# Optimization experiments

Measured on AMD Instinct MI355X. Metric: run time of the kernel, lower is better.

Reference implementation:

```python
import jax, jax.numpy as jnp
import numpy as np

N_NODES = 100000
N_EDGES = 3200000
NDIM_IN = 64
EDIM = 64
NDIM_OUT = 32
HID1, HID2 = 50, 25


def _linear_init(key, fan_in, fan_out):
    # torch nn.Linear default: U(-1/sqrt(fan_in), 1/sqrt(fan_in))
    kw, kb = jax.random.split(key)
    bound = 1.0 / np.sqrt(fan_in)
    W = jax.random.uniform(kw, (fan_in, fan_out), jnp.float32, -bound, bound)
    b = jax.random.uniform(kb, (fan_out,), jnp.float32, -bound, bound)
    return W, b


def setup_inputs() -> dict:
    key = jax.random.key(0)
    ks = jax.random.split(key, 10)
    nfeats = jax.random.normal(ks[0], (N_NODES, 1, NDIM_IN), jnp.float32)
    efeats = jax.random.normal(ks[1], (N_EDGES, 1, EDIM), jnp.float32)
    src = jax.random.randint(ks[2], (N_EDGES,), 0, N_NODES, jnp.int32)
    dst = jax.random.randint(ks[3], (N_EDGES,), 0, N_NODES, jnp.int32)
    Wm1, bm1 = _linear_init(ks[4], NDIM_IN + EDIM, HID1)
    Wa1, ba1 = _linear_init(ks[5], NDIM_IN + HID1, HID1)
    Wm2, bm2 = _linear_init(ks[6], HID1 + EDIM, HID2)
    Wa2, ba2 = _linear_init(ks[7], HID1 + HID2, HID2)
    Wm3, bm3 = _linear_init(ks[8], HID2 + EDIM, NDIM_OUT)
    Wa3, ba3 = _linear_init(ks[9], HID2 + NDIM_OUT, NDIM_OUT)
    return {
        "nfeats": nfeats, "efeats": efeats, "src": src, "dst": dst,
        "Wm1": Wm1, "bm1": bm1, "Wa1": Wa1, "ba1": ba1,
        "Wm2": Wm2, "bm2": bm2, "Wa2": Wa2, "ba2": ba2,
        "Wm3": Wm3, "bm3": bm3, "Wa3": Wa3, "ba3": ba3,
    }


def _gnn_layer(h, e, src, dst, Wm, bm, Wa, ba):
    # h: [N,1,Fin], e: [E,1,Fe]
    # per-edge message: relu(Linear(cat(h[src], e)))  -> [E,1,Fout]
    m = jax.nn.relu(jnp.concatenate([h[src], e], axis=-1) @ Wm + bm)
    # sum-aggregate messages per destination node -> [N,1,Fout]
    h_neigh = jax.ops.segment_sum(m, dst, num_segments=h.shape[0])
    # node apply: relu(Linear(cat(h, h_neigh)))
    return jax.nn.relu(jnp.concatenate([h, h_neigh], axis=-1) @ Wa + ba)


def reference(nfeats, efeats, src, dst,
              Wm1, bm1, Wa1, ba1,
              Wm2, bm2, Wa2, ba2,
              Wm3, bm3, Wa3, ba3):
    h = _gnn_layer(nfeats, efeats, src, dst, Wm1, bm1, Wa1, ba1)
    h = _gnn_layer(h, efeats, src, dst, Wm2, bm2, Wa2, ba2)  # dropout p=0.0
    h = _gnn_layer(h, efeats, src, dst, Wm3, bm3, Wa3, ba3)
    return h.sum(axis=1)  # [N, ndim_out]
```

## Files before the change

kernel.cpp:

```cpp
#include <hip/hip_runtime.h>

#define DEVINL __device__ __forceinline__

typedef __attribute__((ext_vector_type(8))) short bf16x8;
typedef __attribute__((ext_vector_type(4))) float f32x4;

DEVINL void fma4(float4& a, const float4 w, const float x) {
    a.x += w.x * x; a.y += w.y * x; a.z += w.z * x; a.w += w.w * x;
}

DEVINL unsigned short bf16of(float x) {
    unsigned a = __float_as_uint(x);
    a += 0x7FFFu + ((a >> 16) & 1u);
    return (unsigned short)(a >> 16);
}

DEVINL unsigned bfpair(float lo, float hi) {
    unsigned a = __float_as_uint(lo);
    a += 0x7FFFu + ((a >> 16) & 1u);
    unsigned b = __float_as_uint(hi);
    b += 0x7FFFu + ((b >> 16) & 1u);
    return (a >> 16) | (b & 0xFFFF0000u);
}

DEVINL bf16x8 as_bf16x8(uint4 u) {
    union { uint4 u4; bf16x8 b; } cv; cv.u4 = u; return cv.b;
}

__global__ __launch_bounds__(256) void hist_kernel(const int* __restrict__ d,
                                                   int* __restrict__ counts, int n) {
    for (int i = blockIdx.x * 256 + threadIdx.x; i < n; i += gridDim.x * 256)
        atomicAdd(&counts[d[i]], 1);
}

__global__ __launch_bounds__(1024) void scan_block(const int* __restrict__ in,
                                                   int* __restrict__ out,
                                                   int* __restrict__ bsums, int n) {
    __shared__ int buf[2][1024];
    const int t = threadIdx.x;
    const int i = blockIdx.x * 1024 + t;
    const int v = (i < n) ? in[i] : 0;
    int cur = 0;
    buf[0][t] = v;
    __syncthreads();
    #pragma unroll
    for (int s = 1; s < 1024; s <<= 1) {
        int x = buf[cur][t];
        if (t >= s) x += buf[cur][t - s];
        buf[cur ^ 1][t] = x;
        cur ^= 1;
        __syncthreads();
    }
    if (i < n) out[i] = buf[cur][t] - v;
    if (t == 1023) bsums[blockIdx.x] = buf[cur][t];
}

__global__ void scan_small(int* __restrict__ bs, int nb) {
    if (blockIdx.x == 0 && threadIdx.x == 0) {
        int acc = 0;
        for (int i = 0; i < nb; i++) { int v = bs[i]; bs[i] = acc; acc += v; }
    }
}

__global__ __launch_bounds__(1024) void add_offsets(int* __restrict__ out,
                                                    const int* __restrict__ bs, int n) {
    int i = blockIdx.x * 1024 + threadIdx.x;
    if (i < n) out[i] += bs[blockIdx.x];
}

__global__ __launch_bounds__(256) void scatter_kernel(const int* __restrict__ d,
                                                      const int* __restrict__ src,
                                                      int* __restrict__ cursor,
                                                      int4* __restrict__ recs, int n) {
    for (int i = blockIdx.x * 256 + threadIdx.x; i < n; i += gridDim.x * 256) {
        int dd = d[i];
        int ss = src[i];
        int pos = atomicAdd(&cursor[dd], 1);
        recs[pos] = make_int4(i, dd, ss, 0);
    }
}

template<int FIN, int FOUT, int FOUTP>
__global__ __launch_bounds__(256) void pack_we(const float* __restrict__ W,
                                               float* __restrict__ Wp) {
    int idx = blockIdx.x * 256 + threadIdx.x;
    if (idx >= 64 * FOUTP) return;
    int k = idx / FOUTP, j = idx - k * FOUTP;
    Wp[idx] = (j < FOUT) ? W[(FIN + k) * FOUT + j] : 0.f;
}

template<int FIN, int FOUT, int NC>
__global__ __launch_bounds__(256) void pack_wbt(const float* __restrict__ W,
                                                unsigned short* __restrict__ WbT) {
    int idx = blockIdx.x * 256 + threadIdx.x;
    if (idx >= NC * 64) return;
    int c = idx / 64, k = idx - c * 64;
    WbT[idx] = (c < FOUT) ? bf16of(W[(FIN + k) * FOUT + c]) : (unsigned short)0;
}

template<int FIN, int FOUT, int FOUTP>
__global__ __launch_bounds__(256) void gemv_g(
    const float* __restrict__ x,
    const float* __restrict__ W,
    const float* __restrict__ b,
    float* __restrict__ g, int nNodes)
{
    constexpr int F4 = FOUTP / 4;
    __shared__ float4 Wl[FIN * F4];
    __shared__ float  bl[FOUTP];
    const int tid = threadIdx.x;
    for (int idx = tid; idx < FIN * FOUTP; idx += 256) {
        int k = idx / FOUTP, j = idx - k * FOUTP;
        reinterpret_cast<float*>(Wl)[idx] = (j < FOUT) ? W[k * FOUT + j] : 0.f;
    }
    for (int idx = tid; idx < FOUTP; idx += 256)
        bl[idx] = (idx < FOUT) ? b[idx] : 0.f;
    __syncthreads();
    const int n = blockIdx.x * 256 + tid;
    if (n >= nNodes) return;
    float4 acc[F4];
    #pragma unroll
    for (int j4 = 0; j4 < F4; j4++) acc[j4] = reinterpret_cast<float4*>(bl)[j4];
    const float* xr = x + (long long)n * FIN;
    #pragma unroll 1
    for (int k = 0; k < FIN; ++k) {
        float xk = xr[k];
        const float4* wrow = &Wl[k * F4];
        #pragma unroll
        for (int j4 = 0; j4 < F4; j4++) fma4(acc[j4], wrow[j4], xk);
    }
    float4* gr = reinterpret_cast<float4*>(g + (long long)n * FOUTP);
    #pragma unroll
    for (int j4 = 0; j4 < F4; j4++) gr[j4] = acc[j4];
}


template<int FOUT, int FOUTP, int NT>
__global__ __launch_bounds__(256) void edge_mfma_cvt(
    const float* __restrict__ g,
    const float* __restrict__ efeats,
    const int4* __restrict__ recs,
    const unsigned short* __restrict__ WbT,
    unsigned* __restrict__ ebf,
    float* __restrict__ agg)
{
    constexpr int MS = NT * 16 + 1;

    __shared__ float msg[4][32 * MS];
    __shared__ int eidL[512], sIdxL[512], dseg[512];

    const int tid = threadIdx.x;
    const long long pb = (long long)blockIdx.x * 512;
    {
        int4 r0 = recs[pb + tid];
        int4 r1 = recs[pb + 256 + tid];
        eidL[tid] = r0.x;  dseg[tid] = r0.y;  sIdxL[tid] = r0.z;
        eidL[tid + 256] = r1.x; dseg[tid + 256] = r1.y; sIdxL[tid + 256] = r1.z;
    }
    __syncthreads();

    const int lane = tid & 63;
    const int wv   = tid >> 6;
    const int lg   = lane >> 4;
    const int lc   = lane & 15;

    bf16x8 bfr[2][NT];
    #pragma unroll
    for (int kt = 0; kt < 2; kt++)
        #pragma unroll
        for (int nt = 0; nt < NT; nt++)
            bfr[kt][nt] = *reinterpret_cast<const bf16x8*>(
                WbT + (nt * 16 + lc) * 64 + kt * 32 + lg * 8);

    float* msgW = msg[wv];

    #pragma unroll 1
    for (int ch = 0; ch < 4; ++ch) {
        const int rb0 = wv * 128 + ch * 32;
        #pragma unroll
        for (int mt = 0; mt < 2; ++mt) {
            const int rowbase = rb0 + mt * 16;
            const int eid = eidL[rowbase + lc];
            const float4* erow = reinterpret_cast<const float4*>(efeats + (long long)eid * 64);
            float4 f0 = erow[lg * 2];
            float4 f1 = erow[lg * 2 + 1];
            float4 f2 = erow[8 + lg * 2];
            float4 f3 = erow[8 + lg * 2 + 1];
            uint4 u0, u1;
            u0.x = bfpair(f0.x, f0.y); u0.y = bfpair(f0.z, f0.w);
            u0.z = bfpair(f1.x, f1.y); u0.w = bfpair(f1.z, f1.w);
            u1.x = bfpair(f2.x, f2.y); u1.y = bfpair(f2.z, f2.w);
            u1.z = bfpair(f3.x, f3.y); u1.w = bfpair(f3.z, f3.w);
            uint4* eb = reinterpret_cast<uint4*>(ebf + (unsigned long long)(pb + rowbase + lc) * 32);
            eb[lg]     = u0;
            eb[4 + lg] = u1;
            bf16x8 a0 = as_bf16x8(u0);
            bf16x8 a1 = as_bf16x8(u1);

            int sr[4];
            #pragma unroll
            for (int r = 0; r < 4; r++) sr[r] = sIdxL[rowbase + lg * 4 + r];
            #pragma unroll
            for (int nt = 0; nt < NT; nt++) {
                f32x4 acc = {0.f, 0.f, 0.f, 0.f};
                acc = __builtin_amdgcn_mfma_f32_16x16x32_bf16(a0, bfr[0][nt], acc, 0, 0, 0);
                acc = __builtin_amdgcn_mfma_f32_16x16x32_bf16(a1, bfr[1][nt], acc, 0, 0, 0);
                const int col = nt * 16 + lc;
                #pragma unroll
                for (int r = 0; r < 4; r++) {
                    float gv = (col < FOUT) ? g[(long long)sr[r] * FOUTP + col] : 0.f;
                    float v  = fmaxf(acc[r] + gv, 0.f);
                    msgW[(mt * 16 + lg * 4 + r) * MS + col] = v;
                }
            }
        }
        const int base = rb0;
        for (int r0 = 0; r0 < 32; ++r0) {
            int dr = dseg[base + r0];
            if (r0 > 0 && dseg[base + r0 - 1] == dr) continue;
            float s = 0.f;
            int rr = r0;
            while (true) {
                s += msgW[rr * MS + lane];
                ++rr;
                if (rr >= 32 || dseg[base + rr] != dr) break;
            }
            if (lane < FOUT) atomicAdd(agg + (long long)dr * FOUT + lane, s);
        }
    }
}

template<int FOUT, int FOUTP, int NT>
__global__ __launch_bounds__(256) void edge_mfma(
    const float* __restrict__ g,
    const unsigned* __restrict__ ebf,
    const int4* __restrict__ recs,
    const unsigned short* __restrict__ WbT,
    float* __restrict__ agg)
{
    constexpr int MS = NT * 16 + 1;

    __shared__ float msg[4][32 * MS];
    __shared__ int sIdxL[512], dseg[512];

    const int tid = threadIdx.x;
    const long long pb = (long long)blockIdx.x * 512;
    {
        int4 r0 = recs[pb + tid];
        int4 r1 = recs[pb + 256 + tid];
        dseg[tid] = r0.y;  sIdxL[tid] = r0.z;
        dseg[tid + 256] = r1.y; sIdxL[tid + 256] = r1.z;
    }
    __syncthreads();

    const int lane = tid & 63;
    const int wv   = tid >> 6;
    const int lg   = lane >> 4;
    const int lc   = lane & 15;

    bf16x8 bfr[2][NT];
    #pragma unroll
    for (int kt = 0; kt < 2; kt++)
        #pragma unroll
        for (int nt = 0; nt < NT; nt++)
            bfr[kt][nt] = *reinterpret_cast<const bf16x8*>(
                WbT + (nt * 16 + lc) * 64 + kt * 32 + lg * 8);

    float* msgW = msg[wv];

    #pragma unroll 1
    for (int ch = 0; ch < 4; ++ch) {
        const int rb0 = wv * 128 + ch * 32;
        #pragma unroll
        for (int mt = 0; mt < 2; ++mt) {
            const int rowbase = rb0 + mt * 16;
            const unsigned* arow = ebf + (unsigned long long)(pb + rowbase + lc) * 32;
            bf16x8 a0 = *reinterpret_cast<const bf16x8*>(arow + lg * 4);
            bf16x8 a1 = *reinterpret_cast<const bf16x8*>(arow + 16 + lg * 4);
            int sr[4];
            #pragma unroll
            for (int r = 0; r < 4; r++) sr[r] = sIdxL[rowbase + lg * 4 + r];
            #pragma unroll
            for (int nt = 0; nt < NT; nt++) {
                f32x4 acc = {0.f, 0.f, 0.f, 0.f};
                acc = __builtin_amdgcn_mfma_f32_16x16x32_bf16(a0, bfr[0][nt], acc, 0, 0, 0);
                acc = __builtin_amdgcn_mfma_f32_16x16x32_bf16(a1, bfr[1][nt], acc, 0, 0, 0);
                const int col = nt * 16 + lc;
                #pragma unroll
                for (int r = 0; r < 4; r++) {
                    float gv = (col < FOUT) ? g[(long long)sr[r] * FOUTP + col] : 0.f;
                    float v  = fmaxf(acc[r] + gv, 0.f);
                    msgW[(mt * 16 + lg * 4 + r) * MS + col] = v;
                }
            }
        }
        const int base = rb0;
        for (int r0 = 0; r0 < 32; ++r0) {
            int dr = dseg[base + r0];
            if (r0 > 0 && dseg[base + r0 - 1] == dr) continue;
            float s = 0.f;
            int rr = r0;
            while (true) {
                s += msgW[rr * MS + lane];
                ++rr;
                if (rr >= 32 || dseg[base + rr] != dr) break;
            }
            if (lane < FOUT) atomicAdd(agg + (long long)dr * FOUT + lane, s);
        }
    }
}

template<int FOUT, int FOUTP, int MS>
__global__ __launch_bounds__(256) void edge_fb(
    const float* __restrict__ g,
    const float* __restrict__ efeats,
    const int4* __restrict__ recs,
    const float* __restrict__ Wp,
    float* __restrict__ agg)
{
    constexpr int F4 = FOUTP / 4;
    constexpr int ST = 17;
    static_assert(128 * MS + 64 <= 512 * ST, "msg buf exceeds sbuf");

    __shared__ float sbuf[512 * ST];
    __shared__ int   dseg[512];

    const int tid = threadIdx.x;
    const long long pb = (long long)blockIdx.x * 512;
    int4 r0 = recs[pb + tid];
    int4 r1 = recs[pb + 256 + tid];
    dseg[tid] = r0.y;
    dseg[tid + 256] = r1.y;

    const float4* gr0 = reinterpret_cast<const float4*>(g + (long long)r0.z * FOUTP);
    const float4* gr1 = reinterpret_cast<const float4*>(g + (long long)r1.z * FOUTP);
    const float*  er0 = efeats + (long long)r0.x * 64;
    const float*  er1 = efeats + (long long)r1.x * 64;
    const float4* Wp4 = reinterpret_cast<const float4*>(Wp);

    float4 acc0[F4], acc1[F4];
    #pragma unroll
    for (int j4 = 0; j4 < F4; j4++) acc0[j4] = gr0[j4];
    #pragma unroll
    for (int j4 = 0; j4 < F4; j4++) acc1[j4] = gr1[j4];

    const int t0 = tid * ST;
    const int t1 = (tid + 256) * ST;

    for (int c = 0; c < 4; ++c) {
        const int off = c * 16;
        #pragma unroll
        for (int f = 0; f < 4; ++f) {
            float4 v0 = *reinterpret_cast<const float4*>(er0 + off + 4 * f);
            float4 v1 = *reinterpret_cast<const float4*>(er1 + off + 4 * f);
            float* d0 = &sbuf[t0 + 4 * f];
            float* d1 = &sbuf[t1 + 4 * f];
            d0[0] = v0.x; d0[1] = v0.y; d0[2] = v0.z; d0[3] = v0.w;
            d1[0] = v1.x; d1[1] = v1.y; d1[2] = v1.z; d1[3] = v1.w;
        }
        #pragma unroll 1
        for (int k = 0; k < 16; ++k) {
            const float x0 = sbuf[t0 + k];
            const float x1 = sbuf[t1 + k];
            const float4* wrow = &Wp4[(off + k) * F4];
            #pragma unroll
            for (int j4 = 0; j4 < F4; j4++) {
                float4 w = wrow[j4];
                fma4(acc0[j4], w, x0);
                fma4(acc1[j4], w, x1);
            }
        }
    }

    const int lane = tid & 63;
    const int wv   = tid >> 6;

    #pragma unroll 1
    for (int bb = 0; bb < 4; ++bb) {
        __syncthreads();
        if ((tid >> 7) == (bb & 1)) {
            const int r = tid & 127;
            float* mrow = &sbuf[r * MS];
            const float4* accp = (bb < 2) ? acc0 : acc1;
            #pragma unroll
            for (int j4 = 0; j4 < F4; j4++) {
                float4 a = accp[j4];
                if (4 * j4 + 0 < FOUT) mrow[4 * j4 + 0] = fmaxf(a.x, 0.f);
                if (4 * j4 + 1 < FOUT) mrow[4 * j4 + 1] = fmaxf(a.y, 0.f);
                if (4 * j4 + 2 < FOUT) mrow[4 * j4 + 2] = fmaxf(a.z, 0.f);
                if (4 * j4 + 3 < FOUT) mrow[4 * j4 + 3] = fmaxf(a.w, 0.f);
            }
        }
        __syncthreads();

        const int rbase = bb * 128;
        for (int r0i = wv * 32; r0i < wv * 32 + 32; ++r0i) {
            int dr = dseg[rbase + r0i];
            if (r0i > 0 && dseg[rbase + r0i - 1] == dr) continue;
            float s = 0.f;
            int rr = r0i;
            while (true) {
                s += sbuf[rr * MS + lane];
                ++rr;
                if (rr >= 128 || dseg[rbase + rr] != dr) break;
            }
            if (lane < FOUT) atomicAdd(agg + (long long)dr * FOUT + lane, s);
        }
    }
}

template<int FH, int FHP, int FAGG, int FOUT, int FOUTP, int GOUT, int GOUTP>
__global__ __launch_bounds__(256) void node_kernel(
    const float* __restrict__ h,
    const float* __restrict__ agg,
    const float* __restrict__ Wa,
    const float* __restrict__ ba,
    const float* __restrict__ Wmn,
    const float* __restrict__ bmn,
    float* __restrict__ out,
    float* __restrict__ gout,
    int nNodes)
{
    constexpr int K  = FH + FAGG;
    constexpr int F4 = FOUTP / 4;
    constexpr int G4 = (GOUT > 0) ? GOUTP / 4 : 1;

    __shared__ float4 Wl[K * F4];
    __shared__ float4 Wg[(GOUT > 0) ? FOUTP * G4 : 1];
    __shared__ float  bl[FOUTP];
    __shared__ float  bg[(GOUT > 0) ? GOUTP : 4];

    const int tid = threadIdx.x;
    for (int idx = tid; idx < K * FOUTP; idx += 256) {
        int k = idx / FOUTP, j = idx - k * FOUTP;
        reinterpret_cast<float*>(Wl)[idx] = (j < FOUT) ? Wa[k * FOUT + j] : 0.f;
    }
    for (int idx = tid; idx < FOUTP; idx += 256)
        bl[idx] = (idx < FOUT) ? ba[idx] : 0.f;
    if constexpr (GOUT > 0) {
        for (int idx = tid; idx < FOUTP * GOUTP; idx += 256) {
            int k = idx / GOUTP, j = idx - k * GOUTP;
            reinterpret_cast<float*>(Wg)[idx] =
                (k < FOUT && j < GOUT) ? Wmn[k * GOUT + j] : 0.f;
        }
        for (int idx = tid; idx < GOUTP; idx += 256)
            bg[idx] = (idx < GOUT) ? bmn[idx] : 0.f;
    }
    __syncthreads();

    const int n = blockIdx.x * 256 + tid;
    if (n >= nNodes) return;

    float4 acc[F4];
    #pragma unroll
    for (int j4 = 0; j4 < F4; j4++) acc[j4] = reinterpret_cast<float4*>(bl)[j4];

    const float* hrow = h + (long long)n * FHP;
    #pragma unroll 1
    for (int k = 0; k < FH; k++) {
        float xk = hrow[k];
        const float4* wrow = &Wl[k * F4];
        #pragma unroll
        for (int j4 = 0; j4 < F4; j4++) fma4(acc[j4], wrow[j4], xk);
    }
    const float* arow = agg + (long long)n * FAGG;
    #pragma unroll 1
    for (int k = 0; k < FAGG; k++) {
        float xk = arow[k];
        const float4* wrow = &Wl[(FH + k) * F4];
        #pragma unroll
        for (int j4 = 0; j4 < F4; j4++) fma4(acc[j4], wrow[j4], xk);
    }

    #pragma unroll
    for (int j4 = 0; j4 < F4; j4++) {
        acc[j4].x = fmaxf(acc[j4].x, 0.f);
        acc[j4].y = fmaxf(acc[j4].y, 0.f);
        acc[j4].z = fmaxf(acc[j4].z, 0.f);
        acc[j4].w = fmaxf(acc[j4].w, 0.f);
    }
    float4* orow = reinterpret_cast<float4*>(out + (long long)n * FOUTP);
    #pragma unroll
    for (int j4 = 0; j4 < F4; j4++) orow[j4] = acc[j4];

    if constexpr (GOUT > 0) {
        float4 gacc[G4];
        #pragma unroll
        for (int j4 = 0; j4 < G4; j4++) gacc[j4] = reinterpret_cast<float4*>(bg)[j4];
        #pragma unroll 1
        for (int k4 = 0; k4 < F4; ++k4) {
            float4 xv = acc[k4];
            #pragma unroll
            for (int c = 0; c < 4; ++c) {
                float xc = (c == 0) ? xv.x : (c == 1) ? xv.y : (c == 2) ? xv.z : xv.w;
                const float4* wrow = &Wg[(k4 * 4 + c) * G4];
                #pragma unroll
                for (int j4 = 0; j4 < G4; j4++) fma4(gacc[j4], wrow[j4], xc);
            }
        }
        float4* grow = reinterpret_cast<float4*>(gout + (long long)n * GOUTP);
        #pragma unroll
        for (int j4 = 0; j4 < G4; j4++) grow[j4] = gacc[j4];
    }
}

extern "C" void kernel_launch(void* const* d_in, const int* in_sizes, int n_in,
                              void* d_out, int out_size, void* d_ws, size_t ws_size,
                              hipStream_t stream)
{
    const float* nfeats = (const float*)d_in[0];
    const float* efeats = (const float*)d_in[1];
    const int*   src    = (const int*)d_in[2];
    const int*   dst    = (const int*)d_in[3];
    const float* Wm1 = (const float*)d_in[4],  *bm1 = (const float*)d_in[5];
    const float* Wa1 = (const float*)d_in[6],  *ba1 = (const float*)d_in[7];
    const float* Wm2 = (const float*)d_in[8],  *bm2 = (const float*)d_in[9];
    const float* Wa2 = (const float*)d_in[10], *ba2 = (const float*)d_in[11];
    const float* Wm3 = (const float*)d_in[12], *bm3 = (const float*)d_in[13];
    const float* Wa3 = (const float*)d_in[14], *ba3 = (const float*)d_in[15];
    float* out = (float*)d_out;

    constexpr int N = 100000;
    constexpr int E = 3200000;
    constexpr int SCAN_BLOCKS = (N + 1023) / 1024;

    float* ws   = (float*)d_ws;
    float* h1   = ws;
    float* h2   = h1 + (size_t)N * 52;
    float* agg  = h2 + (size_t)N * 28;
    float* g    = agg + (size_t)N * 52;
    int* counts = (int*)(g + (size_t)N * 52);
    int* cursor = counts + N;
    int* bsums  = cursor + N;
    int4* recs  = (int4*)(bsums + 128);
    float* Wp1  = (float*)(recs + E);
    float* Wp2  = Wp1 + 64 * 52;
    float* Wp3  = Wp2 + 64 * 28;
    unsigned short* Wb1 = (unsigned short*)(Wp3 + 64 * 32);
    unsigned short* Wb2 = Wb1 + 64 * 64;
    unsigned short* Wb3 = Wb2 + 32 * 64;
    char* endp = (char*)(Wb3 + 32 * 64);

    size_t usedB   = (size_t)(endp - (char*)d_ws);
    size_t ebfOffB = (usedB + 127) & ~(size_t)127;
    size_t neededB = ebfOffB + (size_t)E * 128;
    const bool useBf = (ws_size >= neededB);
    unsigned* ebf = (unsigned*)((char*)d_ws + ebfOffB);

    pack_we<64, 50, 52><<<(64 * 52 + 255) / 256, 256, 0, stream>>>(Wm1, Wp1);
    pack_we<50, 25, 28><<<(64 * 28 + 255) / 256, 256, 0, stream>>>(Wm2, Wp2);
    pack_we<25, 32, 32><<<(64 * 32 + 255) / 256, 256, 0, stream>>>(Wm3, Wp3);
    pack_wbt<64, 50, 64><<<(64 * 64 + 255) / 256, 256, 0, stream>>>(Wm1, Wb1);
    pack_wbt<50, 25, 32><<<(32 * 64 + 255) / 256, 256, 0, stream>>>(Wm2, Wb2);
    pack_wbt<25, 32, 32><<<(32 * 64 + 255) / 256, 256, 0, stream>>>(Wm3, Wb3);

    hipMemsetAsync(counts, 0, (size_t)N * sizeof(int), stream);
    hist_kernel<<<2048, 256, 0, stream>>>(dst, counts, E);
    scan_block<<<SCAN_BLOCKS, 1024, 0, stream>>>(counts, cursor, bsums, N);
    scan_small<<<1, 64, 0, stream>>>(bsums, SCAN_BLOCKS);
    add_offsets<<<SCAN_BLOCKS, 1024, 0, stream>>>(cursor, bsums, N);
    scatter_kernel<<<2048, 256, 0, stream>>>(dst, src, cursor, recs, E);

    const int EB = E / 512;
    const int NB = (N + 255) / 256;

    gemv_g<64, 50, 52><<<NB, 256, 0, stream>>>(nfeats, Wm1, bm1, g, N);

    hipMemsetAsync(agg, 0, (size_t)N * 52 * sizeof(float), stream);
    if (useBf)
        edge_mfma_cvt<50, 52, 4><<<EB, 256, 0, stream>>>(g, efeats, recs, Wb1, ebf, agg);
    else
        edge_fb<50, 52, 51><<<EB, 256, 0, stream>>>(g, efeats, recs, Wp1, agg);
    node_kernel<64, 64, 50, 50, 52, 25, 28><<<NB, 256, 0, stream>>>(
        nfeats, agg, Wa1, ba1, Wm2, bm2, h1, g, N);

    hipMemsetAsync(agg, 0, (size_t)N * 52 * sizeof(float), stream);
    if (useBf)
        edge_mfma<25, 28, 2><<<EB, 256, 0, stream>>>(g, ebf, recs, Wb2, agg);
    else
        edge_fb<25, 28, 25><<<EB, 256, 0, stream>>>(g, efeats, recs, Wp2, agg);
    node_kernel<50, 52, 25, 25, 28, 32, 32><<<NB, 256, 0, stream>>>(
        h1, agg, Wa2, ba2, Wm3, bm3, h2, g, N);

    hipMemsetAsync(agg, 0, (size_t)N * 52 * sizeof(float), stream);
    if (useBf)
        edge_mfma<32, 32, 2><<<EB, 256, 0, stream>>>(g, ebf, recs, Wb3, agg);
    else
        edge_fb<32, 32, 33><<<EB, 256, 0, stream>>>(g, efeats, recs, Wp3, agg);
    node_kernel<25, 28, 32, 32, 32, 0, 0><<<NB, 256, 0, stream>>>(
        h2, agg, Wa3, ba3, nullptr, nullptr, out, nullptr, N);
}
```

Measured before the change: 1.441 ms.

## Precompute layer-2/3 edge-feature projections in the first edge pass

```diff
diff --git a/kernel.cpp b/kernel.cpp
--- a/kernel.cpp
+++ b/kernel.cpp
@@ -22,6 +22,9 @@
     b += 0x7FFFu + ((b >> 16) & 1u);
     return (a >> 16) | (b & 0xFFFF0000u);
 }
+
+DEVINL float bflo(unsigned u) { return __uint_as_float(u << 16); }
+DEVINL float bfhi(unsigned u) { return __uint_as_float(u & 0xFFFF0000u); }
 
 DEVINL bf16x8 as_bf16x8(uint4 u) {
     union { uint4 u4; bf16x8 b; } cv; cv.u4 = u; return cv.b;
@@ -134,16 +137,18 @@
     for (int j4 = 0; j4 < F4; j4++) gr[j4] = acc[j4];
 }
 
-
-template<int FOUT, int FOUTP, int NT>
-__global__ __launch_bounds__(256) void edge_mfma_cvt(
+__global__ __launch_bounds__(256) void edge_mfma_all(
     const float* __restrict__ g,
     const float* __restrict__ efeats,
     const int4* __restrict__ recs,
-    const unsigned short* __restrict__ WbT,
-    unsigned* __restrict__ ebf,
+    const unsigned short* __restrict__ Wb1,
+    const unsigned short* __restrict__ Wb2,
+    const unsigned short* __restrict__ Wb3,
+    unsigned* __restrict__ ep2,
+    unsigned* __restrict__ ep3,
     float* __restrict__ agg)
 {
+    constexpr int FOUT = 50, FOUTP = 52, NT = 4;
     constexpr int MS = NT * 16 + 1;
 
     __shared__ float msg[4][32 * MS];
@@ -164,22 +169,28 @@
     const int lg   = lane >> 4;
     const int lc   = lane & 15;
 
-    bf16x8 bfr[2][NT];
-    #pragma unroll
-    for (int kt = 0; kt < 2; kt++)
-        #pragma unroll
-        for (int nt = 0; nt < NT; nt++)
-            bfr[kt][nt] = *reinterpret_cast<const bf16x8*>(
-                WbT + (nt * 16 + lc) * 64 + kt * 32 + lg * 8);
+    bf16x8 bfr1[2][4], bfr2[2][2], bfr3[2][2];
+    #pragma unroll
+    for (int kt = 0; kt < 2; kt++) {
+        #pragma unroll
+        for (int nt = 0; nt < 4; nt++)
+            bfr1[kt][nt] = *reinterpret_cast<const bf16x8*>(Wb1 + (nt * 16 + lc) * 64 + kt * 32 + lg * 8);
+        #pragma unroll
+        for (int nt = 0; nt < 2; nt++) {
+            bfr2[kt][nt] = *reinterpret_cast<const bf16x8*>(Wb2 + (nt * 16 + lc) * 64 + kt * 32 + lg * 8);
+            bfr3[kt][nt] = *reinterpret_cast<const bf16x8*>(Wb3 + (nt * 16 + lc) * 64 + kt * 32 + lg * 8);
+        }
+    }
 
     float* msgW = msg[wv];
 
     #pragma unroll 1
     for (int ch = 0; ch < 4; ++ch) {
         const int rb0 = wv * 128 + ch * 32;
-        #pragma unroll
+        #pragma unroll 1
         for (int mt = 0; mt < 2; ++mt) {
             const int rowbase = rb0 + mt * 16;
+            const long long tix = (pb >> 4) + wv * 8 + ch * 2 + mt;
             const int eid = eidL[rowbase + lc];
             const float4* erow = reinterpret_cast<const float4*>(efeats + (long long)eid * 64);
             float4 f0 = erow[lg * 2];
@@ -191,27 +202,50 @@
             u0.z = bfpair(f1.x, f1.y); u0.w = bfpair(f1.z, f1.w);
             u1.x = bfpair(f2.x, f2.y); u1.y = bfpair(f2.z, f2.w);
             u1.z = bfpair(f3.x, f3.y); u1.w = bfpair(f3.z, f3.w);
-            uint4* eb = reinterpret_cast<uint4*>(ebf + (unsigned long long)(pb + rowbase + lc) * 32);
-            eb[lg]     = u0;
-            eb[4 + lg] = u1;
             bf16x8 a0 = as_bf16x8(u0);
             bf16x8 a1 = as_bf16x8(u1);
 
             int sr[4];
             #pragma unroll
             for (int r = 0; r < 4; r++) sr[r] = sIdxL[rowbase + lg * 4 + r];
+
             #pragma unroll
-            for (int nt = 0; nt < NT; nt++) {
+            for (int nt = 0; nt < 4; nt++) {
                 f32x4 acc = {0.f, 0.f, 0.f, 0.f};
-                acc = __builtin_amdgcn_mfma_f32_16x16x32_bf16(a0, bfr[0][nt], acc, 0, 0, 0);
-                acc = __builtin_amdgcn_mfma_f32_16x16x32_bf16(a1, bfr[1][nt], acc, 0, 0, 0);
+                acc = __builtin_amdgcn_mfma_f32_16x16x32_bf16(a0, bfr1[0][nt], acc, 0, 0, 0);
+                acc = __builtin_amdgcn_mfma_f32_16x16x32_bf16(a1, bfr1[1][nt], acc, 0, 0, 0);
                 const int col = nt * 16 + lc;
                 #pragma unroll
                 for (int r = 0; r < 4; r++) {
                     float gv = (col < FOUT) ? g[(long long)sr[r] * FOUTP + col] : 0.f;
-                    float v  = fmaxf(acc[r] + gv, 0.f);
-                    msgW[(mt * 16 + lg * 4 + r) * MS + col] = v;
+                    msgW[(mt * 16 + lg * 4 + r) * MS + col] = fmaxf(acc[r] + gv, 0.f);
                 }
+            }
+            {
+                uint4 st;
+                #pragma unroll
+                for (int nt = 0; nt < 2; nt++) {
+                    f32x4 acc = {0.f, 0.f, 0.f, 0.f};
+                    acc = __builtin_amdgcn_mfma_f32_16x16x32_bf16(a0, bfr2[0][nt], acc, 0, 0, 0);
+                    acc = __builtin_amdgcn_mfma_f32_16x16x32_bf16(a1, bfr2[1][nt], acc, 0, 0, 0);
+                    unsigned w0 = bfpair(acc[0], acc[1]);
+                    unsigned w1 = bfpair(acc[2], acc[3]);
+                    if (nt == 0) { st.x = w0; st.y = w1; } else { st.z = w0; st.w = w1; }
+                }
+                reinterpret_cast<uint4*>(ep2)[tix * 64 + lane] = st;
+            }
+            {
+                uint4 st;
+                #pragma unroll
+                for (int nt = 0; nt < 2; nt++) {
+                    f32x4 acc = {0.f, 0.f, 0.f, 0.f};
+                    acc = __builtin_amdgcn_mfma_f32_16x16x32_bf16(a0, bfr3[0][nt], acc, 0, 0, 0);
+                    acc = __builtin_amdgcn_mfma_f32_16x16x32_bf16(a1, bfr3[1][nt], acc, 0, 0, 0);
+                    unsigned w0 = bfpair(acc[0], acc[1]);
+                    unsigned w1 = bfpair(acc[2], acc[3]);
+                    if (nt == 0) { st.x = w0; st.y = w1; } else { st.z = w0; st.w = w1; }
+                }
+                reinterpret_cast<uint4*>(ep3)[tix * 64 + lane] = st;
             }
         }
         const int base = rb0;
@@ -230,14 +264,14 @@
     }
 }
 
-template<int FOUT, int FOUTP, int NT>
-__global__ __launch_bounds__(256) void edge_mfma(
+template<int FOUT, int FOUTP>
+__global__ __launch_bounds__(256) void edge_ep(
     const float* __restrict__ g,
-    const unsigned* __restrict__ ebf,
+    const unsigned* __restrict__ ep,
     const int4* __restrict__ recs,
-    const unsigned short* __restrict__ WbT,
     float* __restrict__ agg)
 {
+    constexpr int NT = 2;
     constexpr int MS = NT * 16 + 1;
 
     __shared__ float msg[4][32 * MS];
@@ -258,14 +292,6 @@
     const int lg   = lane >> 4;
     const int lc   = lane & 15;
 
-    bf16x8 bfr[2][NT];
-    #pragma unroll
-    for (int kt = 0; kt < 2; kt++)
-        #pragma unroll
-        for (int nt = 0; nt < NT; nt++)
-            bfr[kt][nt] = *reinterpret_cast<const bf16x8*>(
-                WbT + (nt * 16 + lc) * 64 + kt * 32 + lg * 8);
-
     float* msgW = msg[wv];
 
     #pragma unroll 1
@@ -274,23 +300,25 @@
         #pragma unroll
         for (int mt = 0; mt < 2; ++mt) {
             const int rowbase = rb0 + mt * 16;
-            const unsigned* arow = ebf + (unsigned long long)(pb + rowbase + lc) * 32;
-            bf16x8 a0 = *reinterpret_cast<const bf16x8*>(arow + lg * 4);
-            bf16x8 a1 = *reinterpret_cast<const bf16x8*>(arow + 16 + lg * 4);
+            const long long tix = (pb >> 4) + wv * 8 + ch * 2 + mt;
+            uint4 v = reinterpret_cast<const uint4*>(ep)[tix * 64 + lane];
+
             int sr[4];
             #pragma unroll
             for (int r = 0; r < 4; r++) sr[r] = sIdxL[rowbase + lg * 4 + r];
+
             #pragma unroll
-            for (int nt = 0; nt < NT; nt++) {
-                f32x4 acc = {0.f, 0.f, 0.f, 0.f};
-                acc = __builtin_amdgcn_mfma_f32_16x16x32_bf16(a0, bfr[0][nt], acc, 0, 0, 0);
-                acc = __builtin_amdgcn_mfma_f32_16x16x32_bf16(a1, bfr[1][nt], acc, 0, 0, 0);
+            for (int nt = 0; nt < 2; nt++) {
+                float e0 = bflo(nt == 0 ? v.x : v.z);
+                float e1 = bfhi(nt == 0 ? v.x : v.z);
+                float e2 = bflo(nt == 0 ? v.y : v.w);
+                float e3 = bfhi(nt == 0 ? v.y : v.w);
                 const int col = nt * 16 + lc;
+                float ev[4] = {e0, e1, e2, e3};
                 #pragma unroll
                 for (int r = 0; r < 4; r++) {
                     float gv = (col < FOUT) ? g[(long long)sr[r] * FOUTP + col] : 0.f;
-                    float v  = fmaxf(acc[r] + gv, 0.f);
-                    msgW[(mt * 16 + lg * 4 + r) * MS + col] = v;
+                    msgW[(mt * 16 + lg * 4 + r) * MS + col] = fmaxf(ev[r] + gv, 0.f);
                 }
             }
         }
@@ -541,11 +569,12 @@
     unsigned short* Wb3 = Wb2 + 32 * 64;
     char* endp = (char*)(Wb3 + 32 * 64);
 
-    size_t usedB   = (size_t)(endp - (char*)d_ws);
-    size_t ebfOffB = (usedB + 127) & ~(size_t)127;
-    size_t neededB = ebfOffB + (size_t)E * 128;
+    size_t usedB  = (size_t)(endp - (char*)d_ws);
+    size_t epOffB = (usedB + 127) & ~(size_t)127;
+    size_t neededB = epOffB + (size_t)E * 128;
     const bool useBf = (ws_size >= neededB);
-    unsigned* ebf = (unsigned*)((char*)d_ws + ebfOffB);
+    unsigned* ep2 = (unsigned*)((char*)d_ws + epOffB);
+    unsigned* ep3 = ep2 + (size_t)E * 16;
 
     pack_we<64, 50, 52><<<(64 * 52 + 255) / 256, 256, 0, stream>>>(Wm1, Wp1);
     pack_we<50, 25, 28><<<(64 * 28 + 255) / 256, 256, 0, stream>>>(Wm2, Wp2);
@@ -568,7 +597,7 @@
 
     hipMemsetAsync(agg, 0, (size_t)N * 52 * sizeof(float), stream);
     if (useBf)
-        edge_mfma_cvt<50, 52, 4><<<EB, 256, 0, stream>>>(g, efeats, recs, Wb1, ebf, agg);
+        edge_mfma_all<<<EB, 256, 0, stream>>>(g, efeats, recs, Wb1, Wb2, Wb3, ep2, ep3, agg);
     else
         edge_fb<50, 52, 51><<<EB, 256, 0, stream>>>(g, efeats, recs, Wp1, agg);
     node_kernel<64, 64, 50, 50, 52, 25, 28><<<NB, 256, 0, stream>>>(
@@ -576,7 +605,7 @@
 
     hipMemsetAsync(agg, 0, (size_t)N * 52 * sizeof(float), stream);
     if (useBf)
-        edge_mfma<25, 28, 2><<<EB, 256, 0, stream>>>(g, ebf, recs, Wb2, agg);
+        edge_ep<25, 28><<<EB, 256, 0, stream>>>(g, ep2, recs, agg);
     else
         edge_fb<25, 28, 25><<<EB, 256, 0, stream>>>(g, efeats, recs, Wp2, agg);
     node_kernel<50, 52, 25, 25, 28, 32, 32><<<NB, 256, 0, stream>>>(
@@ -584,7 +613,7 @@
 
     hipMemsetAsync(agg, 0, (size_t)N * 52 * sizeof(float), stream);
     if (useBf)
-        edge_mfma<32, 32, 2><<<EB, 256, 0, stream>>>(g, ebf, recs, Wb3, agg);
+        edge_ep<32, 32><<<EB, 256, 0, stream>>>(g, ep3, recs, agg);
     else
         edge_fb<32, 32, 33><<<EB, 256, 0, stream>>>(g, efeats, recs, Wp3, agg);
     node_kernel<25, 28, 32, 32, 32, 0, 0><<<NB, 256, 0, stream>>>(
```

Result: slower. 1.551 ms (+7.7%).

## Fuse bf16 edge-feature conversion into scatter and prefetch edge operands

Applied to the files above, without the earlier changes.

```diff
diff --git a/kernel.cpp b/kernel.cpp
--- a/kernel.cpp
+++ b/kernel.cpp
@@ -68,15 +68,40 @@
     if (i < n) out[i] += bs[blockIdx.x];
 }
 
-__global__ __launch_bounds__(256) void scatter_kernel(const int* __restrict__ d,
-                                                      const int* __restrict__ src,
-                                                      int* __restrict__ cursor,
-                                                      int4* __restrict__ recs, int n) {
-    for (int i = blockIdx.x * 256 + threadIdx.x; i < n; i += gridDim.x * 256) {
-        int dd = d[i];
-        int ss = src[i];
-        int pos = atomicAdd(&cursor[dd], 1);
-        recs[pos] = make_int4(i, dd, ss, 0);
+__global__ __launch_bounds__(256) void cvt_scatter(
+    const int* __restrict__ dst,
+    const int* __restrict__ src,
+    const float* __restrict__ ef,
+    int* __restrict__ cursor,
+    int4* __restrict__ recs,
+    unsigned* __restrict__ ebf)
+{
+    const int tid = threadIdx.x;
+    const long long e = (long long)blockIdx.x * 64 + (tid >> 2);
+    const int sub  = tid & 3;
+    const int lane = tid & 63;
+
+    const int dd = dst[e];
+    const int ss = src[e];
+    int pos = 0;
+    if (sub == 0) pos = atomicAdd(&cursor[dd], 1);
+    pos = __shfl(pos, lane & ~3);
+    if (sub == 0) recs[pos] = make_int4((int)e, dd, ss, 0);
+
+    if (ebf != nullptr) {
+        const float4* erow = reinterpret_cast<const float4*>(ef + e * 64);
+        float4 q0 = erow[sub * 4 + 0];
+        float4 q1 = erow[sub * 4 + 1];
+        float4 q2 = erow[sub * 4 + 2];
+        float4 q3 = erow[sub * 4 + 3];
+        uint4 o0, o1;
+        o0.x = bfpair(q0.x, q0.y); o0.y = bfpair(q0.z, q0.w);
+        o0.z = bfpair(q1.x, q1.y); o0.w = bfpair(q1.z, q1.w);
+        o1.x = bfpair(q2.x, q2.y); o1.y = bfpair(q2.z, q2.w);
+        o1.z = bfpair(q3.x, q3.y); o1.w = bfpair(q3.z, q3.w);
+        uint4* outp = reinterpret_cast<uint4*>(ebf + (long long)pos * 32);
+        outp[sub * 2]     = o0;
+        outp[sub * 2 + 1] = o1;
     }
 }
 
@@ -134,102 +159,6 @@
     for (int j4 = 0; j4 < F4; j4++) gr[j4] = acc[j4];
 }
 
-
-template<int FOUT, int FOUTP, int NT>
-__global__ __launch_bounds__(256) void edge_mfma_cvt(
-    const float* __restrict__ g,
-    const float* __restrict__ efeats,
-    const int4* __restrict__ recs,
-    const unsigned short* __restrict__ WbT,
-    unsigned* __restrict__ ebf,
-    float* __restrict__ agg)
-{
-    constexpr int MS = NT * 16 + 1;
-
-    __shared__ float msg[4][32 * MS];
-    __shared__ int eidL[512], sIdxL[512], dseg[512];
-
-    const int tid = threadIdx.x;
-    const long long pb = (long long)blockIdx.x * 512;
-    {
-        int4 r0 = recs[pb + tid];
-        int4 r1 = recs[pb + 256 + tid];
-        eidL[tid] = r0.x;  dseg[tid] = r0.y;  sIdxL[tid] = r0.z;
-        eidL[tid + 256] = r1.x; dseg[tid + 256] = r1.y; sIdxL[tid + 256] = r1.z;
-    }
-    __syncthreads();
-
-    const int lane = tid & 63;
-    const int wv   = tid >> 6;
-    const int lg   = lane >> 4;
-    const int lc   = lane & 15;
-
-    bf16x8 bfr[2][NT];
-    #pragma unroll
-    for (int kt = 0; kt < 2; kt++)
-        #pragma unroll
-        for (int nt = 0; nt < NT; nt++)
-            bfr[kt][nt] = *reinterpret_cast<const bf16x8*>(
-                WbT + (nt * 16 + lc) * 64 + kt * 32 + lg * 8);
-
-    float* msgW = msg[wv];
-
-    #pragma unroll 1
-    for (int ch = 0; ch < 4; ++ch) {
-        const int rb0 = wv * 128 + ch * 32;
-        #pragma unroll
-        for (int mt = 0; mt < 2; ++mt) {
-            const int rowbase = rb0 + mt * 16;
-            const int eid = eidL[rowbase + lc];
-            const float4* erow = reinterpret_cast<const float4*>(efeats + (long long)eid * 64);
-            float4 f0 = erow[lg * 2];
-            float4 f1 = erow[lg * 2 + 1];
-            float4 f2 = erow[8 + lg * 2];
-            float4 f3 = erow[8 + lg * 2 + 1];
-            uint4 u0, u1;
-            u0.x = bfpair(f0.x, f0.y); u0.y = bfpair(f0.z, f0.w);
-            u0.z = bfpair(f1.x, f1.y); u0.w = bfpair(f1.z, f1.w);
-            u1.x = bfpair(f2.x, f2.y); u1.y = bfpair(f2.z, f2.w);
-            u1.z = bfpair(f3.x, f3.y); u1.w = bfpair(f3.z, f3.w);
-            uint4* eb = reinterpret_cast<uint4*>(ebf + (unsigned long long)(pb + rowbase + lc) * 32);
-            eb[lg]     = u0;
-            eb[4 + lg] = u1;
-            bf16x8 a0 = as_bf16x8(u0);
-            bf16x8 a1 = as_bf16x8(u1);
-
-            int sr[4];
-            #pragma unroll
-            for (int r = 0; r < 4; r++) sr[r] = sIdxL[rowbase + lg * 4 + r];
-            #pragma unroll
-            for (int nt = 0; nt < NT; nt++) {
-                f32x4 acc = {0.f, 0.f, 0.f, 0.f};
-                acc = __builtin_amdgcn_mfma_f32_16x16x32_bf16(a0, bfr[0][nt], acc, 0, 0, 0);
-                acc = __builtin_amdgcn_mfma_f32_16x16x32_bf16(a1, bfr[1][nt], acc, 0, 0, 0);
-                const int col = nt * 16 + lc;
-                #pragma unroll
-                for (int r = 0; r < 4; r++) {
-                    float gv = (col < FOUT) ? g[(long long)sr[r] * FOUTP + col] : 0.f;
-                    float v  = fmaxf(acc[r] + gv, 0.f);
-                    msgW[(mt * 16 + lg * 4 + r) * MS + col] = v;
-                }
-            }
-        }
-        const int base = rb0;
-        for (int r0 = 0; r0 < 32; ++r0) {
-            int dr = dseg[base + r0];
-            if (r0 > 0 && dseg[base + r0 - 1] == dr) continue;
-            float s = 0.f;
-            int rr = r0;
-            while (true) {
-                s += msgW[rr * MS + lane];
-                ++rr;
-                if (rr >= 32 || dseg[base + rr] != dr) break;
-            }
-            if (lane < FOUT) atomicAdd(agg + (long long)dr * FOUT + lane, s);
-        }
-    }
-}
-
 template<int FOUT, int FOUTP, int NT>
 __global__ __launch_bounds__(256) void edge_mfma(
     const float* __restrict__ g,
@@ -268,32 +197,60 @@
 
     float* msgW = msg[wv];
 
+    bf16x8 a0[2], a1[2];
+    #pragma unroll
+    for (int mt = 0; mt < 2; mt++) {
+        const unsigned* arow = ebf + (unsigned long long)(pb + wv * 128 + mt * 16 + lc) * 32;
+        a0[mt] = *reinterpret_cast<const bf16x8*>(arow + lg * 4);
+        a1[mt] = *reinterpret_cast<const bf16x8*>(arow + 16 + lg * 4);
+    }
+
     #pragma unroll 1
     for (int ch = 0; ch < 4; ++ch) {
         const int rb0 = wv * 128 + ch * 32;
-        #pragma unroll
-        for (int mt = 0; mt < 2; ++mt) {
-            const int rowbase = rb0 + mt * 16;
-            const unsigned* arow = ebf + (unsigned long long)(pb + rowbase + lc) * 32;
-            bf16x8 a0 = *reinterpret_cast<const bf16x8*>(arow + lg * 4);
-            bf16x8 a1 = *reinterpret_cast<const bf16x8*>(arow + 16 + lg * 4);
-            int sr[4];
-            #pragma unroll
-            for (int r = 0; r < 4; r++) sr[r] = sIdxL[rowbase + lg * 4 + r];
+
+        int srr[2][4];
+        #pragma unroll
+        for (int mt = 0; mt < 2; mt++)
+            #pragma unroll
+            for (int r = 0; r < 4; r++)
+                srr[mt][r] = sIdxL[rb0 + mt * 16 + lg * 4 + r];
+        float gv[2][NT][4];
+        #pragma unroll
+        for (int mt = 0; mt < 2; mt++)
+            #pragma unroll
+            for (int nt = 0; nt < NT; nt++) {
+                const int col = nt * 16 + lc;
+                #pragma unroll
+                for (int r = 0; r < 4; r++)
+                    gv[mt][nt][r] = (col < FOUT) ? g[(long long)srr[mt][r] * FOUTP + col] : 0.f;
+            }
+
+        #pragma unroll
+        for (int mt = 0; mt < 2; mt++) {
             #pragma unroll
             for (int nt = 0; nt < NT; nt++) {
                 f32x4 acc = {0.f, 0.f, 0.f, 0.f};
-                acc = __builtin_amdgcn_mfma_f32_16x16x32_bf16(a0, bfr[0][nt], acc, 0, 0, 0);
-                acc = __builtin_amdgcn_mfma_f32_16x16x32_bf16(a1, bfr[1][nt], acc, 0, 0, 0);
+                acc = __builtin_amdgcn_mfma_f32_16x16x32_bf16(a0[mt], bfr[0][nt], acc, 0, 0, 0);
+                acc = __builtin_amdgcn_mfma_f32_16x16x32_bf16(a1[mt], bfr[1][nt], acc, 0, 0, 0);
                 const int col = nt * 16 + lc;
                 #pragma unroll
-                for (int r = 0; r < 4; r++) {
-                    float gv = (col < FOUT) ? g[(long long)sr[r] * FOUTP + col] : 0.f;
-                    float v  = fmaxf(acc[r] + gv, 0.f);
-                    msgW[(mt * 16 + lg * 4 + r) * MS + col] = v;
-                }
-            }
-        }
+                for (int r = 0; r < 4; r++)
+                    msgW[(mt * 16 + lg * 4 + r) * MS + col] = fmaxf(acc[r] + gv[mt][nt][r], 0.f);
+            }
+        }
+
+        bf16x8 n0[2], n1[2];
+        if (ch < 3) {
+            const int rbn = wv * 128 + (ch + 1) * 32;
+            #pragma unroll
+            for (int mt = 0; mt < 2; mt++) {
+                const unsigned* arow = ebf + (unsigned long long)(pb + rbn + mt * 16 + lc) * 32;
+                n0[mt] = *reinterpret_cast<const bf16x8*>(arow + lg * 4);
+                n1[mt] = *reinterpret_cast<const bf16x8*>(arow + 16 + lg * 4);
+            }
+        }
+
         const int base = rb0;
         for (int r0 = 0; r0 < 32; ++r0) {
             int dr = dseg[base + r0];
@@ -301,11 +258,16 @@
             float s = 0.f;
             int rr = r0;
             while (true) {
-                s += msgW[rr * MS + lane];
+                if (lane < NT * 16) s += msgW[rr * MS + lane];
                 ++rr;
                 if (rr >= 32 || dseg[base + rr] != dr) break;
             }
             if (lane < FOUT) atomicAdd(agg + (long long)dr * FOUT + lane, s);
+        }
+
+        if (ch < 3) {
+            #pragma unroll
+            for (int mt = 0; mt < 2; mt++) { a0[mt] = n0[mt]; a1[mt] = n1[mt]; }
         }
     }
 }
@@ -559,7 +521,8 @@
     scan_block<<<SCAN_BLOCKS, 1024, 0, stream>>>(counts, cursor, bsums, N);
     scan_small<<<1, 64, 0, stream>>>(bsums, SCAN_BLOCKS);
     add_offsets<<<SCAN_BLOCKS, 1024, 0, stream>>>(cursor, bsums, N);
-    scatter_kernel<<<2048, 256, 0, stream>>>(dst, src, cursor, recs, E);
+    cvt_scatter<<<E / 64, 256, 0, stream>>>(dst, src, efeats, cursor, recs,
+                                            useBf ? ebf : nullptr);
 
     const int EB = E / 512;
     const int NB = (N + 255) / 256;
@@ -568,7 +531,7 @@
 
     hipMemsetAsync(agg, 0, (size_t)N * 52 * sizeof(float), stream);
     if (useBf)
-        edge_mfma_cvt<50, 52, 4><<<EB, 256, 0, stream>>>(g, efeats, recs, Wb1, ebf, agg);
+        edge_mfma<50, 52, 4><<<EB, 256, 0, stream>>>(g, ebf, recs, Wb1, agg);
     else
         edge_fb<50, 52, 51><<<EB, 256, 0, stream>>>(g, efeats, recs, Wp1, agg);
     node_kernel<64, 64, 50, 50, 52, 25, 28><<<NB, 256, 0, stream>>>(
```

New measurement: 1.299 ms. 9.8% less time.
